# Kernel tuning notes

Measured on AMD Instinct MI355X. Metric: run time of the kernel, lower is better.

Reference implementation:

```python
import jax, jax.numpy as jnp
import numpy as np

EPS = 1e-5
NUM_GRAPHS = 64


def _linear(x, W, b):
    return x @ W + b


def setup_inputs() -> dict:
    key = jax.random.key(0)
    ks = jax.random.split(key, 32)
    N, E, IN, EF, H, ED, T, L, C = 25000, 400000, 128, 16, 32, 32, 4, 2, 1
    F = H            # F_in (divide_input=False)
    Fo = H // T      # F_out per tower

    def w(k, shape):
        return jax.random.normal(k, shape, jnp.float32) / np.sqrt(shape[-2])

    inp = {
        'x': jax.random.normal(ks[0], (N, IN), jnp.float32),
        'edge_attr': jax.random.normal(ks[1], (E, EF), jnp.float32),
        'edge_weight': jax.random.uniform(ks[2], (E,), jnp.float32),
        'edge_index': jax.random.randint(ks[3], (2, E), 0, N),
        'batch': jnp.sort(jax.random.randint(ks[4], (N,), 0, NUM_GRAPHS)),
        'node_W': w(ks[5], (IN, H)), 'node_b': jnp.zeros((H,), jnp.float32),
        'edge_W': w(ks[6], (EF, ED)), 'edge_b': jnp.zeros((ED,), jnp.float32),
        'enc_W': w(ks[7], (L, ED, F)), 'enc_b': jnp.zeros((L, F), jnp.float32),
        'pre_W': w(ks[8], (L, T, 3 * F, F)), 'pre_b': jnp.zeros((L, T, F), jnp.float32),
        'post_W': w(ks[9], (L, T, 13 * F, Fo)), 'post_b': jnp.zeros((L, T, Fo), jnp.float32),
        'lin_W': w(ks[10], (L, H, H)), 'lin_b': jnp.zeros((L, H), jnp.float32),
        'bn_g': jnp.ones((L, H), jnp.float32), 'bn_b': jnp.zeros((L, H), jnp.float32),
        'mlp_W1': w(ks[11], (H, H)), 'mlp_b1': jnp.zeros((H,), jnp.float32),
        'mlp_W2': w(ks[12], (H, H // 2)), 'mlp_b2': jnp.zeros((H // 2,), jnp.float32),
        'mlp_W3': w(ks[13], (H // 2, C)), 'mlp_b3': jnp.zeros((C,), jnp.float32),
    }
    return inp


def reference(x, edge_attr, edge_weight, node_W, node_b, edge_W, edge_b,
              enc_W, enc_b, pre_W, pre_b, post_W, post_b, lin_W, lin_b,
              bn_g, bn_b, mlp_W1, mlp_b1, mlp_W2, mlp_b2, mlp_W3, mlp_b3,
              edge_index, batch):
    N = x.shape[0]
    L, T = pre_W.shape[0], pre_W.shape[1]
    src, dst = edge_index[0], edge_index[1]

    # degree-based scalers (PNA): avg_deg_log = mean_n log(deg_n + 1)
    deg = jax.ops.segment_sum(jnp.ones((src.shape[0],), x.dtype), dst, num_segments=N)
    avg_deg_log = jnp.mean(jnp.log(deg + 1.0))
    degc = jnp.clip(deg, 1.0)[:, None, None]          # [N,1,1]
    log_deg = jnp.log(degc + 1.0)
    amp = log_deg / avg_deg_log                        # amplification scaler
    att = avg_deg_log / log_deg                        # attenuation scaler
    has_edge = (deg > 0)[:, None, None]

    h = _linear(x, node_W, node_b)                     # node_emb  [N,H]
    e = _linear(edge_attr, edge_W, edge_b)             # edge_emb  [E,ED]

    for l in range(L):
        el = _linear(e, enc_W[l], enc_b[l])            # edge_encoder [E,F]
        m_in = jnp.concatenate([h[dst], h[src], el], axis=-1)      # [E,3F]
        msg = jnp.einsum('ef,tfg->etg', m_in, pre_W[l]) + pre_b[l]  # per-tower pre_nn [E,T,F]
        msg = msg * edge_weight[:, None, None]
        s = jax.ops.segment_sum(msg, dst, num_segments=N)
        s2 = jax.ops.segment_sum(msg * msg, dst, num_segments=N)
        mean = s / degc
        std = jnp.sqrt(jax.nn.relu(s2 / degc - mean * mean) + EPS)
        mn = jnp.where(has_edge, jax.ops.segment_min(msg, dst, num_segments=N), 0.0)
        mx = jnp.where(has_edge, jax.ops.segment_max(msg, dst, num_segments=N), 0.0)
        agg = jnp.concatenate([mean, mn, mx, std], axis=-1)            # [N,T,4F]
        agg = jnp.concatenate([agg, agg * amp, agg * att], axis=-1)    # [N,T,12F]
        out = jnp.concatenate(
            [jnp.broadcast_to(h[:, None, :], (N, T, h.shape[-1])), agg], axis=-1)  # [N,T,13F]
        out = jnp.einsum('ntf,tfg->ntg', out, post_W[l]) + post_b[l]   # post_nn [N,T,Fo]
        out = out.reshape(N, -1) @ lin_W[l] + lin_b[l]                 # [N,H]
        mu = jnp.mean(out, axis=0)
        var = jnp.var(out, axis=0)
        out = (out - mu) / jnp.sqrt(var + EPS) * bn_g[l] + bn_b[l]     # BatchNorm (batch stats)
        h = jax.nn.relu(out)

    g = jax.ops.segment_sum(h, batch, num_segments=NUM_GRAPHS)        # global_add_pool
    g = jax.nn.relu(_linear(g, mlp_W1, mlp_b1))
    g = jax.nn.relu(_linear(g, mlp_W2, mlp_b2))
    return _linear(g, mlp_W3, mlp_b3)
```

## Files before the change

kernel.cpp:

```cpp
#include <hip/hip_runtime.h>

constexpr float kEps = 1e-5f;

typedef _Float16 h2 __attribute__((ext_vector_type(2)));

__device__ __forceinline__ unsigned short f2bf(float x) {
  unsigned int u = __float_as_uint(x);
  unsigned int r = (u + 0x7fffu + ((u >> 16) & 1u)) >> 16;
  return (unsigned short)r;
}
__device__ __forceinline__ float bflo(unsigned int u) { return __uint_as_float(u << 16); }
__device__ __forceinline__ float bfhi(unsigned int u) { return __uint_as_float(u & 0xffff0000u); }
__device__ __forceinline__ unsigned int packbf(float a, float b) {
  return (unsigned int)f2bf(a) | ((unsigned int)f2bf(b) << 16);
}
__device__ __forceinline__ unsigned int pkh2(float a, float b) {
  h2 v; v.x = (_Float16)a; v.y = (_Float16)b;
  return __builtin_bit_cast(unsigned int, v);
}
__device__ __forceinline__ float dot2a(h2 a, h2 b, float c) {
#if __has_builtin(__builtin_amdgcn_fdot2)
  return __builtin_amdgcn_fdot2(a, b, c, false);
#else
  return c + (float)a.x * (float)b.x + (float)a.y * (float)b.y;
#endif
}
__device__ __forceinline__ h2 ash2(unsigned int u) { return __builtin_bit_cast(h2, u); }


__global__ void zero_kernel(int* __restrict__ a, int* __restrict__ b,
                            float* __restrict__ bnb, int n) {
  int i = blockIdx.x * blockDim.x + threadIdx.x;
  if (i < n) { a[i] = 0; b[i] = 0; }
  if (i < 128) bnb[i] = 0.f;
}

__global__ void hist_kernel(const int* __restrict__ dst, int* __restrict__ deg, int E) {
  int e = blockIdx.x * blockDim.x + threadIdx.x;
  if (e < E) atomicAdd(&deg[dst[e]], 1);
}

__global__ void scan1_kernel(const int* __restrict__ deg, int* __restrict__ off,
                             int* __restrict__ part, int N) {
  __shared__ int sm[1024];
  int i = blockIdx.x * 1024 + threadIdx.x;
  int v = (i < N) ? deg[i] : 0;
  sm[threadIdx.x] = v;
  __syncthreads();
  for (int o = 1; o < 1024; o <<= 1) {
    int t = (threadIdx.x >= o) ? sm[threadIdx.x - o] : 0;
    __syncthreads();
    sm[threadIdx.x] += t;
    __syncthreads();
  }
  if (i < N) off[i] = sm[threadIdx.x] - v;
  if (threadIdx.x == 1023) part[blockIdx.x] = sm[1023];
}

__global__ void scan2_kernel(int* __restrict__ part, int* __restrict__ off, int nb, int N) {
  if (threadIdx.x == 0) {
    int run = 0;
    for (int b = 0; b < nb; b++) { int p = part[b]; part[b] = run; run += p; }
    off[N] = run;
  }
}

__global__ void scan3_kernel(int* __restrict__ off, const int* __restrict__ part, int N) {
  int i = blockIdx.x * 1024 + threadIdx.x;
  if (i < N) off[i] += part[blockIdx.x];
}

__global__ void fill_kernel(const int* __restrict__ src, const int* __restrict__ dst,
                            const float* __restrict__ ew, const float4* __restrict__ eattr4,
                            const int* __restrict__ off, int* __restrict__ cnt,
                            int* __restrict__ srcs, float* __restrict__ ews,
                            uint4* __restrict__ eg16, int E) {
  int e = blockIdx.x * blockDim.x + threadIdx.x;
  if (e < E) {
    int d = dst[e];
    int slot = off[d] + atomicAdd(&cnt[d], 1);
    srcs[slot] = src[e];
    ews[slot] = ew[e];
    float4 a = eattr4[e * 4 + 0], b = eattr4[e * 4 + 1];
    float4 c = eattr4[e * 4 + 2], q = eattr4[e * 4 + 3];
    uint4 u0, u1;
    u0.x = pkh2(a.x, a.y); u0.y = pkh2(a.z, a.w);
    u0.z = pkh2(b.x, b.y); u0.w = pkh2(b.z, b.w);
    u1.x = pkh2(c.x, c.y); u1.y = pkh2(c.z, c.w);
    u1.z = pkh2(q.x, q.y); u1.w = pkh2(q.z, q.w);
    eg16[(size_t)slot * 2 + 0] = u0;
    eg16[(size_t)slot * 2 + 1] = u1;
  }
}

__global__ void adl_kernel(const int* __restrict__ deg, float* __restrict__ adl, int N) {
  __shared__ float sm[1024];
  float s = 0.f;
  for (int n = threadIdx.x; n < N; n += 1024) s += logf((float)deg[n] + 1.f);
  sm[threadIdx.x] = s;
  __syncthreads();
  for (int o = 512; o > 0; o >>= 1) {
    if (threadIdx.x < o) sm[threadIdx.x] += sm[threadIdx.x + o];
    __syncthreads();
  }
  if (threadIdx.x == 0) adl[0] = sm[0];
}

__global__ void node_emb_kernel(const float* __restrict__ x, const float* __restrict__ W,
                                const float* __restrict__ b, float* __restrict__ h, int N) {
  int n = blockIdx.x * 8 + (threadIdx.x >> 5);
  int j = threadIdx.x & 31;
  if (n >= N) return;
  float acc = b[j];
  const float4* x4 = (const float4*)(x + (size_t)n * 128);
#pragma unroll
  for (int q = 0; q < 32; q++) {
    float4 v = x4[q];
    acc += v.x * W[(4 * q + 0) * 32 + j];
    acc += v.y * W[(4 * q + 1) * 32 + j];
    acc += v.z * W[(4 * q + 2) * 32 + j];
    acc += v.w * W[(4 * q + 3) * 32 + j];
  }
  h[n * 32 + j] = acc;
}

__global__ void fuse_kernel(const float* __restrict__ edge_W, const float* __restrict__ edge_b,
                            const float* __restrict__ enc_W, const float* __restrict__ enc_b,
                            const float* __restrict__ pre_W, const float* __restrict__ pre_b,
                            float* __restrict__ Wf, float* __restrict__ bf) {
  __shared__ float tW[2][16][32];
  __shared__ float tb[2][32];
  int tid = threadIdx.x;
  for (int i = tid; i < 1024; i += 256) {
    int l = i >> 9, r = (i >> 5) & 15, c = i & 31;
    float s = 0.f;
    for (int k = 0; k < 32; k++) s += edge_W[r * 32 + k] * enc_W[(l * 32 + k) * 32 + c];
    tW[l][r][c] = s;
  }
  for (int i = tid; i < 64; i += 256) {
    int l = i >> 5, c = i & 31;
    float s = enc_b[l * 32 + c];
    for (int k = 0; k < 32; k++) s += edge_b[k] * enc_W[(l * 32 + k) * 32 + c];
    tb[l][c] = s;
  }
  __syncthreads();
  for (int i = tid; i < 4096; i += 256) {
    int l = i >> 11, t = (i >> 9) & 3, r = (i >> 5) & 15, c = i & 31;
    float s = 0.f;
    for (int k = 0; k < 32; k++) s += tW[l][r][k] * pre_W[((l * 4 + t) * 96 + 64 + k) * 32 + c];
    Wf[i] = s;
  }
  for (int i = tid; i < 256; i += 256) {
    int l = i >> 7, t = (i >> 5) & 3, c = i & 31;
    float s = pre_b[(l * 4 + t) * 32 + c];
    for (int k = 0; k < 32; k++) s += tb[l][k] * pre_W[((l * 4 + t) * 96 + 64 + k) * 32 + c];
    bf[i] = s;
  }
}

__global__ __launch_bounds__(256) void prep_kernel(
    const float* __restrict__ h, const float* __restrict__ preW,
    const float* __restrict__ bfv, unsigned short* __restrict__ qB,
    unsigned short* __restrict__ AB, int N) {
  __shared__ float hs[16][32];
  int tid = threadIdx.x;
  int c = tid & 127, half = tid >> 7;
  int t = c >> 5, g = c & 31;
  float ws[32], wd[32];
  {
    const float* pS = preW + (t * 96 + 32) * 32 + g;
    const float* pD = preW + (t * 96) * 32 + g;
#pragma unroll
    for (int k = 0; k < 32; k++) { ws[k] = pS[k * 32]; wd[k] = pD[k * 32]; }
  }
  float bc = bfv[c];
  int base = blockIdx.x * 16;
  for (int i = tid; i < 512; i += 256) {
    int nn = i >> 5;
    hs[nn][i & 31] = (base + nn < N) ? h[(size_t)(base + nn) * 32 + (i & 31)] : 0.f;
  }
  __syncthreads();
#pragma unroll
  for (int nn = 0; nn < 8; ++nn) {
    int nl = half + 2 * nn;
    int n = base + nl;
    if (n >= N) continue;
    float qa = 0.f, Aa = bc;
#pragma unroll
    for (int k = 0; k < 32; k++) {
      float hk = hs[nl][k];
      qa = fmaf(hk, ws[k], qa);
      Aa = fmaf(hk, wd[k], Aa);
    }
    qB[(size_t)n * 128 + c] = f2bf(qa);
    AB[(size_t)n * 128 + c] = f2bf(Aa);
  }
}

__global__ __launch_bounds__(256) void bnprep_kernel(
    const float* __restrict__ pre, const float* __restrict__ bnv,
    const float* __restrict__ gamma, const float* __restrict__ beta,
    const float* __restrict__ preW, const float* __restrict__ bfv,
    float* __restrict__ h, unsigned short* __restrict__ qB,
    unsigned short* __restrict__ AB, int N) {
  __shared__ float hs[16][32];
  int tid = threadIdx.x;
  int base = blockIdx.x * 16;
  float invN = 1.f / (float)N;
  for (int idx = tid; idx < 512; idx += 256) {
    int nn = idx >> 5, j = idx & 31;
    int n = base + nn;
    float v = 0.f;
    if (n < N) {
      float mu = bnv[j] * invN;
      float var = bnv[32 + j] * invN - mu * mu;
      float is = rsqrtf(var + kEps);
      v = fmaxf((pre[(size_t)n * 32 + j] - mu) * is * gamma[j] + beta[j], 0.f);
      h[(size_t)n * 32 + j] = v;
    }
    hs[nn][j] = v;
  }
  int c = tid & 127, half = tid >> 7;
  int t = c >> 5, g = c & 31;
  float ws[32], wd[32];
  {
    const float* pS = preW + (t * 96 + 32) * 32 + g;
    const float* pD = preW + (t * 96) * 32 + g;
#pragma unroll
    for (int k = 0; k < 32; k++) { ws[k] = pS[k * 32]; wd[k] = pD[k * 32]; }
  }
  float bc = bfv[c];
  __syncthreads();
#pragma unroll
  for (int nn = 0; nn < 8; ++nn) {
    int nl = half + 2 * nn;
    int n = base + nl;
    if (n >= N) continue;
    float qa = 0.f, Aa = bc;
#pragma unroll
    for (int k = 0; k < 32; k++) {
      float hk = hs[nl][k];
      qa = fmaf(hk, ws[k], qa);
      Aa = fmaf(hk, wd[k], Aa);
    }
    qB[(size_t)n * 128 + c] = f2bf(qa);
    AB[(size_t)n * 128 + c] = f2bf(Aa);
  }
}

#define DOTE(F0, F1, UA, UB)                                         \
  F0 = dot2a(ash2(UA.x), w0[0], F0); F1 = dot2a(ash2(UA.x), w1[0], F1); \
  F0 = dot2a(ash2(UA.y), w0[1], F0); F1 = dot2a(ash2(UA.y), w1[1], F1); \
  F0 = dot2a(ash2(UA.z), w0[2], F0); F1 = dot2a(ash2(UA.z), w1[2], F1); \
  F0 = dot2a(ash2(UA.w), w0[3], F0); F1 = dot2a(ash2(UA.w), w1[3], F1); \
  F0 = dot2a(ash2(UB.x), w0[4], F0); F1 = dot2a(ash2(UB.x), w1[4], F1); \
  F0 = dot2a(ash2(UB.y), w0[5], F0); F1 = dot2a(ash2(UB.y), w1[5], F1); \
  F0 = dot2a(ash2(UB.z), w0[6], F0); F1 = dot2a(ash2(UB.z), w1[6], F1); \
  F0 = dot2a(ash2(UB.w), w0[7], F0); F1 = dot2a(ash2(UB.w), w1[7], F1);

#define STATACC(V0, V1)                                                    \
  s0a += V0; sq0 = fmaf(V0, V0, sq0); mn0 = fminf(mn0, V0); mx0 = fmaxf(mx0, V0); \
  s1a += V1; sq1 = fmaf(V1, V1, sq1); mn1 = fminf(mn1, V1); mx1 = fmaxf(mx1, V1);

__global__ __launch_bounds__(256, 4) void agg8_kernel(
    const unsigned int* __restrict__ qB, const unsigned int* __restrict__ AB,
    const int* __restrict__ coff, const int* __restrict__ srcs,
    const float* __restrict__ ews, const uint4* __restrict__ eg16,
    const float* __restrict__ Wf, unsigned int* __restrict__ stats, int N) {
  int lane = threadIdx.x & 63;
  int n = (blockIdx.x * blockDim.x + threadIdx.x) >> 6;
  if (n >= N) return;
  int t = lane >> 4, g0 = (2 * lane) & 31;
  h2 w0[8], w1[8];
  {
    const float* p = Wf + t * 512 + g0;
#pragma unroll
    for (int k = 0; k < 8; k++) {
      w0[k].x = (_Float16)p[(2 * k) * 32];     w0[k].y = (_Float16)p[(2 * k + 1) * 32];
      w1[k].x = (_Float16)p[(2 * k) * 32 + 1]; w1[k].y = (_Float16)p[(2 * k + 1) * 32 + 1];
    }
  }
  unsigned int au = AB[(size_t)n * 64 + lane];
  float a0 = bflo(au), a1 = bfhi(au);
  int beg = coff[n], end = coff[n + 1];
  int dg = end - beg;
  float s0a = 0.f, s1a = 0.f, sq0 = 0.f, sq1 = 0.f;
  float mn0 = 1e30f, mn1 = 1e30f, mx0 = -1e30f, mx1 = -1e30f;

  int i = beg;
  int sc0 = 0, sc1 = 0, sc2 = 0, sc3 = 0;
  if (i + 4 <= end) { sc0 = srcs[i]; sc1 = srcs[i + 1]; sc2 = srcs[i + 2]; sc3 = srcs[i + 3]; }
  for (; i + 4 <= end; i += 4) {
    unsigned int q0 = qB[(size_t)sc0 * 64 + lane];
    unsigned int q1 = qB[(size_t)sc1 * 64 + lane];
    unsigned int q2 = qB[(size_t)sc2 * 64 + lane];
    unsigned int q3 = qB[(size_t)sc3 * 64 + lane];
    float w0s = ews[i], w1s = ews[i + 1], w2s = ews[i + 2], w3s = ews[i + 3];
    const uint4* ep = eg16 + (size_t)i * 2;
    uint4 eA0 = ep[0], eA1 = ep[1], eB0 = ep[2], eB1 = ep[3];
    uint4 eC0 = ep[4], eC1 = ep[5], eD0 = ep[6], eD1 = ep[7];
    if (i + 8 <= end) { sc0 = srcs[i + 4]; sc1 = srcs[i + 5]; sc2 = srcs[i + 6]; sc3 = srcs[i + 7]; }
    float f00 = 0.f, f10 = 0.f, f01 = 0.f, f11 = 0.f;
    float f02 = 0.f, f12 = 0.f, f03 = 0.f, f13 = 0.f;
    DOTE(f00, f10, eA0, eA1)
    DOTE(f01, f11, eB0, eB1)
    DOTE(f02, f12, eC0, eC1)
    DOTE(f03, f13, eD0, eD1)
    float v0, v1;
    v0 = (a0 + bflo(q0) + f00) * w0s; v1 = (a1 + bfhi(q0) + f10) * w0s; STATACC(v0, v1)
    v0 = (a0 + bflo(q1) + f01) * w1s; v1 = (a1 + bfhi(q1) + f11) * w1s; STATACC(v0, v1)
    v0 = (a0 + bflo(q2) + f02) * w2s; v1 = (a1 + bfhi(q2) + f12) * w2s; STATACC(v0, v1)
    v0 = (a0 + bflo(q3) + f03) * w3s; v1 = (a1 + bfhi(q3) + f13) * w3s; STATACC(v0, v1)
  }
  for (; i < end; ++i) {
    int s = srcs[i];
    unsigned int q = qB[(size_t)s * 64 + lane];
    float w = ews[i];
    const uint4* ep = eg16 + (size_t)i * 2;
    uint4 ea = ep[0], eb = ep[1];
    float f0 = 0.f, f1 = 0.f;
    DOTE(f0, f1, ea, eb)
    float v0 = (a0 + bflo(q) + f0) * w;
    float v1 = (a1 + bfhi(q) + f1) * w;
    STATACC(v0, v1)
  }
  if (dg == 0) { mn0 = 0.f; mx0 = 0.f; mn1 = 0.f; mx1 = 0.f; }
  float inv = 1.f / (float)(dg > 0 ? dg : 1);
  float mean0 = s0a * inv, mean1 = s1a * inv;
  float sd0 = sqrtf(fmaxf(sq0 * inv - mean0 * mean0, 0.f) + kEps);
  float sd1 = sqrtf(fmaxf(sq1 * inv - mean1 * mean1, 0.f) + kEps);
  unsigned int* sp = stats + (size_t)n * 256;
  sp[0 * 64 + lane] = packbf(mean0, mean1);
  sp[1 * 64 + lane] = packbf(mn0, mn1);
  sp[2 * 64 + lane] = packbf(mx0, mx1);
  sp[3 * 64 + lane] = packbf(sd0, sd1);
}

__global__ __launch_bounds__(256) void post_kernel(
    const float* __restrict__ h, const unsigned int* __restrict__ stats,
    const int* __restrict__ coff, const float* __restrict__ adl,
    const float* __restrict__ postW, const float* __restrict__ postB,
    const float* __restrict__ linW, const float* __restrict__ linB,
    float* __restrict__ pre, float* __restrict__ bn, int N) {
  __shared__ unsigned int pwp[208 * 32];
  __shared__ unsigned int stu[4][256];
  __shared__ float red[8][32];
  int tid = threadIdx.x;
  for (int i = tid; i < 6656; i += 256) {
    int r = i >> 5, cc = i & 31, tP = cc >> 3, gq = cc & 7;
    float lo = postW[tP * 3328 + (2 * r) * 8 + gq];
    float hi = postW[tP * 3328 + (2 * r + 1) * 8 + gq];
    pwp[i] = packbf(lo, hi);
  }
  __syncthreads();

  int wave = tid >> 6, lane = tid & 63;
  int c = lane & 31, hh = lane >> 5;
  int tP = c >> 3;
  float adN = adl[0];
  float bs = 0.f, bq = 0.f;

  for (int n = blockIdx.x * 4 + wave; n < N; n += gridDim.x * 4) {
    {
      uint4 su = ((const uint4*)stats)[(size_t)n * 64 + lane];
      ((uint4*)stu[wave])[lane] = su;
    }
    int dg = coff[n + 1] - coff[n];
    float degc = (float)(dg > 0 ? dg : 1);
    float ad = adN / (float)N;
    float ld = logf(degc + 1.f);
    float amp = ld / ad, att = ad / ld;

    float acc = (hh == 0) ? postB[tP * 8 + (c & 7)] : 0.f;
    const float4* h4 = (const float4*)(h + (size_t)n * 32);
#pragma unroll
    for (int q4 = 0; q4 < 4; q4++) {
      float4 hv = h4[hh * 4 + q4];
      int r0 = hh * 8 + q4 * 2;
      unsigned int u0 = pwp[r0 * 32 + c], u1 = pwp[(r0 + 1) * 32 + c];
      acc = fmaf(hv.x, bflo(u0), acc);
      acc = fmaf(hv.y, bfhi(u0), acc);
      acc = fmaf(hv.z, bflo(u1), acc);
      acc = fmaf(hv.w, bfhi(u1), acc);
    }
#pragma unroll 8
    for (int jj = 0; jj < 32; jj++) {
      int sIdx = hh * 2 + (jj >> 4);
      unsigned int sv = stu[wave][sIdx * 64 + tP * 16 + (jj & 15)];
      float v0 = bflo(sv), v1 = bfhi(sv);
      int rm = 16 + hh * 32 + jj, ra = 80 + hh * 32 + jj, rt = 144 + hh * 32 + jj;
      unsigned int um = pwp[rm * 32 + c];
      unsigned int ua = pwp[ra * 32 + c];
      unsigned int ut = pwp[rt * 32 + c];
      float w0 = bflo(um); w0 = fmaf(amp, bflo(ua), w0); w0 = fmaf(att, bflo(ut), w0);
      float w1 = bfhi(um); w1 = fmaf(amp, bfhi(ua), w1); w1 = fmaf(att, bfhi(ut), w1);
      acc = fmaf(v0, w0, acc);
      acc = fmaf(v1, w1, acc);
    }
    acc += __shfl_xor(acc, 32);
    float o = linB[c];
#pragma unroll
    for (int k = 0; k < 32; k++) {
      float a = __shfl(acc, k);
      o = fmaf(a, linW[k * 32 + c], o);
    }
    if (lane < 32) {
      pre[(size_t)n * 32 + c] = o;
      bs += o;
      bq = fmaf(o, o, bq);
    }
  }

  __syncthreads();
  if (lane < 32) {
    red[wave * 2 + 0][c] = bs;
    red[wave * 2 + 1][c] = bq;
  }
  __syncthreads();
  if (tid < 64) {
    int which = tid >> 5, cc = tid & 31;
    float s = red[0 * 2 + which][cc] + red[1 * 2 + which][cc] +
              red[2 * 2 + which][cc] + red[3 * 2 + which][cc];
    atomicAdd(&bn[which * 32 + cc], s);
  }
}


__device__ __forceinline__ int lower_bound_dev(const int* a, int n, int key) {
  int lo = 0, hi = n;
  while (lo < hi) {
    int m = (lo + hi) >> 1;
    if (a[m] < key) lo = m + 1; else hi = m;
  }
  return lo;
}

__global__ void pool2_kernel(const float* __restrict__ pre, const float* __restrict__ bnv,
                             const float* __restrict__ gamma, const float* __restrict__ beta,
                             const int* __restrict__ batch, float* __restrict__ gp, int N) {
  int gi = blockIdx.x;
  int lo = lower_bound_dev(batch, N, gi);
  int hi = lower_bound_dev(batch, N, gi + 1);
  __shared__ float part[8][32];
  int j = threadIdx.x & 31, ch = threadIdx.x >> 5;
  float invN = 1.f / (float)N;
  float mu = bnv[j] * invN;
  float var = bnv[32 + j] * invN - mu * mu;
  float is = rsqrtf(var + kEps);
  float gm = gamma[j], bt = beta[j];
  float s = 0.f;
  for (int n = lo + ch; n < hi; n += 8)
    s += fmaxf((pre[(size_t)n * 32 + j] - mu) * is * gm + bt, 0.f);
  part[ch][j] = s;
  __syncthreads();
  if (threadIdx.x < 32) {
    float t = 0.f;
    for (int c2 = 0; c2 < 8; c2++) t += part[c2][j];
    gp[gi * 32 + j] = t;
  }
}

__global__ void mlp_kernel(const float* __restrict__ gp,
                           const float* __restrict__ W1, const float* __restrict__ b1,
                           const float* __restrict__ W2, const float* __restrict__ b2,
                           const float* __restrict__ W3, const float* __restrict__ b3,
                           float* __restrict__ out) {
  __shared__ float g1[64 * 32];
  __shared__ float g2[64 * 16];
  int tid = threadIdx.x;
  for (int i = tid; i < 2048; i += 256) {
    int r = i >> 5, c = i & 31;
    float s = b1[c];
    for (int k = 0; k < 32; k++) s += gp[r * 32 + k] * W1[k * 32 + c];
    g1[i] = fmaxf(s, 0.f);
  }
  __syncthreads();
  for (int i = tid; i < 1024; i += 256) {
    int r = i >> 4, c = i & 15;
    float s = b2[c];
    for (int k = 0; k < 32; k++) s += g1[r * 32 + k] * W2[k * 16 + c];
    g2[i] = fmaxf(s, 0.f);
  }
  __syncthreads();
  if (tid < 64) {
    float s = b3[0];
    for (int k = 0; k < 16; k++) s += g2[tid * 16 + k] * W3[k];
    out[tid] = s;
  }
}


extern "C" void kernel_launch(void* const* d_in, const int* in_sizes, int n_in,
                              void* d_out, int out_size, void* d_ws, size_t ws_size,
                              hipStream_t stream) {
  (void)n_in; (void)out_size; (void)ws_size;
  const float* x     = (const float*)d_in[0];
  const float* eattr = (const float*)d_in[1];
  const float* ew    = (const float*)d_in[2];
  const int*   eidx  = (const int*)d_in[3];
  const int*   batch = (const int*)d_in[4];
  const float* nodeW = (const float*)d_in[5];
  const float* nodeB = (const float*)d_in[6];
  const float* edgeW = (const float*)d_in[7];
  const float* edgeB = (const float*)d_in[8];
  const float* encW  = (const float*)d_in[9];
  const float* encB  = (const float*)d_in[10];
  const float* preW  = (const float*)d_in[11];
  const float* preB  = (const float*)d_in[12];
  const float* postW = (const float*)d_in[13];
  const float* postB = (const float*)d_in[14];
  const float* linW  = (const float*)d_in[15];
  const float* linB  = (const float*)d_in[16];
  const float* bnG   = (const float*)d_in[17];
  const float* bnB   = (const float*)d_in[18];
  const float* W1    = (const float*)d_in[19];
  const float* b1    = (const float*)d_in[20];
  const float* W2    = (const float*)d_in[21];
  const float* b2    = (const float*)d_in[22];
  const float* W3    = (const float*)d_in[23];
  const float* b3    = (const float*)d_in[24];
  float* out = (float*)d_out;

  int N = in_sizes[0] / 128;
  int E = in_sizes[2];
  const int* srcp = eidx;
  const int* dstp = eidx + E;

  char* wsb = (char*)d_ws;
  size_t woff = 0;
  auto alloc = [&](size_t bytes) -> void* {
    void* p = (void*)(wsb + woff);
    woff += (bytes + 255) & ~(size_t)255;
    return p;
  };
  int* deg   = (int*)alloc((size_t)N * 4);
  int* cnt   = (int*)alloc((size_t)N * 4);
  int* coff  = (int*)alloc((size_t)(N + 1) * 4);
  int* part  = (int*)alloc(64 * 4);
  int* srcs  = (int*)alloc((size_t)E * 4);
  float* ews = (float*)alloc((size_t)E * 4);
  unsigned int* eg16 = (unsigned int*)alloc((size_t)E * 32);
  float* h    = (float*)alloc((size_t)N * 32 * 4);
  float* pre  = (float*)alloc((size_t)N * 32 * 4);
  float* adl  = (float*)alloc(256);
  float* bnbuf = (float*)alloc(2 * 64 * 4);
  float* gp   = (float*)alloc(64 * 32 * 4);
  float* WfB  = (float*)alloc(2 * 4 * 16 * 32 * 4);
  float* bfB  = (float*)alloc(2 * 4 * 32 * 4);
  unsigned short* qB  = (unsigned short*)alloc((size_t)N * 128 * 2);
  unsigned short* AB  = (unsigned short*)alloc((size_t)N * 128 * 2);
  unsigned int* stats = (unsigned int*)alloc((size_t)N * 256 * 4);

  int nb = (N + 1023) / 1024;
  zero_kernel<<<(N + 255) / 256, 256, 0, stream>>>(deg, cnt, bnbuf, N);
  hist_kernel<<<(E + 255) / 256, 256, 0, stream>>>(dstp, deg, E);
  scan1_kernel<<<nb, 1024, 0, stream>>>(deg, coff, part, N);
  scan2_kernel<<<1, 64, 0, stream>>>(part, coff, nb, N);
  scan3_kernel<<<nb, 1024, 0, stream>>>(coff, part, N);
  fill_kernel<<<(E + 255) / 256, 256, 0, stream>>>(srcp, dstp, ew, (const float4*)eattr,
                                                   coff, cnt, srcs, ews, (uint4*)eg16, E);
  adl_kernel<<<1, 1024, 0, stream>>>(deg, adl, N);
  node_emb_kernel<<<(N + 7) / 8, 256, 0, stream>>>(x, nodeW, nodeB, h, N);
  fuse_kernel<<<1, 256, 0, stream>>>(edgeW, edgeB, encW, encB, preW, preB, WfB, bfB);

  prep_kernel<<<(N + 15) / 16, 256, 0, stream>>>(h, preW, bfB, qB, AB, N);
  agg8_kernel<<<(N + 3) / 4, 256, 0, stream>>>(
      (const unsigned int*)qB, (const unsigned int*)AB, coff, srcs, ews,
      (const uint4*)eg16, WfB, stats, N);
  post_kernel<<<1280, 256, 0, stream>>>(
      h, stats, coff, adl, postW, postB, linW, linB, pre, bnbuf, N);
  bnprep_kernel<<<(N + 15) / 16, 256, 0, stream>>>(
      pre, bnbuf, bnG, bnB, preW + 12288, bfB + 128, h, qB, AB, N);
  agg8_kernel<<<(N + 3) / 4, 256, 0, stream>>>(
      (const unsigned int*)qB, (const unsigned int*)AB, coff, srcs, ews,
      (const uint4*)eg16, WfB + 2048, stats, N);
  post_kernel<<<1280, 256, 0, stream>>>(
      h, stats, coff, adl, postW + 13312, postB + 32, linW + 1024, linB + 32,
      pre, bnbuf + 64, N);
  pool2_kernel<<<64, 256, 0, stream>>>(pre, bnbuf + 64, bnG + 32, bnB + 32, batch, gp, N);
  mlp_kernel<<<1, 256, 0, stream>>>(gp, W1, b1, W2, b2, W3, b3, out);
}
```

Measured before the change: 388.6 us.

## Prefetch neighbor rows one iteration ahead and pack post-kernel scaler FMAs

The aggregation kernel now issues the gathers of source-node rows for the next group of four edges before computing the current group, and fetches source indices two groups ahead. The aim is to hide gather latency behind the edge dot-product math. The post kernel keeps three packed two-wide accumulators (mean, amplified, attenuated) and applies the amp and att scalers once at the end instead of per term, which cuts per-iteration FMAs. Its grid is also halved. The prefetch raises register pressure and the reordered sums can change rounding slightly.

```diff
diff --git a/kernel.cpp b/kernel.cpp
--- a/kernel.cpp
+++ b/kernel.cpp
@@ -3,6 +3,7 @@
 constexpr float kEps = 1e-5f;
 
 typedef _Float16 h2 __attribute__((ext_vector_type(2)));
+typedef float f2v __attribute__((ext_vector_type(2)));
 
 __device__ __forceinline__ unsigned short f2bf(float x) {
   unsigned int u = __float_as_uint(x);
@@ -26,6 +27,8 @@
 #endif
 }
 __device__ __forceinline__ h2 ash2(unsigned int u) { return __builtin_bit_cast(h2, u); }
+__device__ __forceinline__ f2v fma2(f2v a, f2v b, f2v c) { return __builtin_elementwise_fma(a, b, c); }
+__device__ __forceinline__ f2v unbf2(unsigned int u) { f2v r; r.x = bflo(u); r.y = bfhi(u); return r; }
 
 
 __global__ void zero_kernel(int* __restrict__ a, int* __restrict__ b,
@@ -262,7 +265,7 @@
   s0a += V0; sq0 = fmaf(V0, V0, sq0); mn0 = fminf(mn0, V0); mx0 = fmaxf(mx0, V0); \
   s1a += V1; sq1 = fmaf(V1, V1, sq1); mn1 = fminf(mn1, V1); mx1 = fmaxf(mx1, V1);
 
-__global__ __launch_bounds__(256, 4) void agg8_kernel(
+__global__ __launch_bounds__(256, 4) void agg9_kernel(
     const unsigned int* __restrict__ qB, const unsigned int* __restrict__ AB,
     const int* __restrict__ coff, const int* __restrict__ srcs,
     const float* __restrict__ ews, const uint4* __restrict__ eg16,
@@ -288,18 +291,29 @@
   float mn0 = 1e30f, mn1 = 1e30f, mx0 = -1e30f, mx1 = -1e30f;
 
   int i = beg;
+  unsigned int q0 = 0, q1 = 0, q2 = 0, q3 = 0;
   int sc0 = 0, sc1 = 0, sc2 = 0, sc3 = 0;
-  if (i + 4 <= end) { sc0 = srcs[i]; sc1 = srcs[i + 1]; sc2 = srcs[i + 2]; sc3 = srcs[i + 3]; }
+  if (i + 4 <= end) {
+    int t0 = srcs[i], t1 = srcs[i + 1], t2 = srcs[i + 2], t3 = srcs[i + 3];
+    q0 = qB[(size_t)t0 * 64 + lane];
+    q1 = qB[(size_t)t1 * 64 + lane];
+    q2 = qB[(size_t)t2 * 64 + lane];
+    q3 = qB[(size_t)t3 * 64 + lane];
+  }
+  if (i + 8 <= end) { sc0 = srcs[i + 4]; sc1 = srcs[i + 5]; sc2 = srcs[i + 6]; sc3 = srcs[i + 7]; }
   for (; i + 4 <= end; i += 4) {
-    unsigned int q0 = qB[(size_t)sc0 * 64 + lane];
-    unsigned int q1 = qB[(size_t)sc1 * 64 + lane];
-    unsigned int q2 = qB[(size_t)sc2 * 64 + lane];
-    unsigned int q3 = qB[(size_t)sc3 * 64 + lane];
+    unsigned int nq0 = 0, nq1 = 0, nq2 = 0, nq3 = 0;
+    if (i + 8 <= end) {
+      nq0 = qB[(size_t)sc0 * 64 + lane];
+      nq1 = qB[(size_t)sc1 * 64 + lane];
+      nq2 = qB[(size_t)sc2 * 64 + lane];
+      nq3 = qB[(size_t)sc3 * 64 + lane];
+    }
     float w0s = ews[i], w1s = ews[i + 1], w2s = ews[i + 2], w3s = ews[i + 3];
     const uint4* ep = eg16 + (size_t)i * 2;
     uint4 eA0 = ep[0], eA1 = ep[1], eB0 = ep[2], eB1 = ep[3];
     uint4 eC0 = ep[4], eC1 = ep[5], eD0 = ep[6], eD1 = ep[7];
-    if (i + 8 <= end) { sc0 = srcs[i + 4]; sc1 = srcs[i + 5]; sc2 = srcs[i + 6]; sc3 = srcs[i + 7]; }
+    if (i + 12 <= end) { sc0 = srcs[i + 8]; sc1 = srcs[i + 9]; sc2 = srcs[i + 10]; sc3 = srcs[i + 11]; }
     float f00 = 0.f, f10 = 0.f, f01 = 0.f, f11 = 0.f;
     float f02 = 0.f, f12 = 0.f, f03 = 0.f, f13 = 0.f;
     DOTE(f00, f10, eA0, eA1)
@@ -311,6 +325,7 @@
     v0 = (a0 + bflo(q1) + f01) * w1s; v1 = (a1 + bfhi(q1) + f11) * w1s; STATACC(v0, v1)
     v0 = (a0 + bflo(q2) + f02) * w2s; v1 = (a1 + bfhi(q2) + f12) * w2s; STATACC(v0, v1)
     v0 = (a0 + bflo(q3) + f03) * w3s; v1 = (a1 + bfhi(q3) + f13) * w3s; STATACC(v0, v1)
+    q0 = nq0; q1 = nq1; q2 = nq2; q3 = nq3;
   }
   for (; i < end; ++i) {
     int s = srcs[i];
@@ -383,20 +398,24 @@
       acc = fmaf(hv.z, bflo(u1), acc);
       acc = fmaf(hv.w, bfhi(u1), acc);
     }
+    f2v ym, ya, yt;
+    ym.x = 0.f; ym.y = 0.f; ya = ym; yt = ym;
 #pragma unroll 8
     for (int jj = 0; jj < 32; jj++) {
       int sIdx = hh * 2 + (jj >> 4);
       unsigned int sv = stu[wave][sIdx * 64 + tP * 16 + (jj & 15)];
-      float v0 = bflo(sv), v1 = bfhi(sv);
-      int rm = 16 + hh * 32 + jj, ra = 80 + hh * 32 + jj, rt = 144 + hh * 32 + jj;
-      unsigned int um = pwp[rm * 32 + c];
-      unsigned int ua = pwp[ra * 32 + c];
-      unsigned int ut = pwp[rt * 32 + c];
-      float w0 = bflo(um); w0 = fmaf(amp, bflo(ua), w0); w0 = fmaf(att, bflo(ut), w0);
-      float w1 = bfhi(um); w1 = fmaf(amp, bfhi(ua), w1); w1 = fmaf(att, bfhi(ut), w1);
-      acc = fmaf(v0, w0, acc);
-      acc = fmaf(v1, w1, acc);
-    }
+      f2v v2 = unbf2(sv);
+      int rm = 16 + hh * 32 + jj;
+      f2v um = unbf2(pwp[rm * 32 + c]);
+      f2v ua = unbf2(pwp[(rm + 64) * 32 + c]);
+      f2v ut = unbf2(pwp[(rm + 128) * 32 + c]);
+      ym = fma2(v2, um, ym);
+      ya = fma2(v2, ua, ya);
+      yt = fma2(v2, ut, yt);
+    }
+    acc += ym.x + ym.y;
+    acc = fmaf(amp, ya.x + ya.y, acc);
+    acc = fmaf(att, yt.x + yt.y, acc);
     acc += __shfl_xor(acc, 32);
     float o = linB[c];
 #pragma unroll
@@ -564,17 +583,17 @@
   fuse_kernel<<<1, 256, 0, stream>>>(edgeW, edgeB, encW, encB, preW, preB, WfB, bfB);
 
   prep_kernel<<<(N + 15) / 16, 256, 0, stream>>>(h, preW, bfB, qB, AB, N);
-  agg8_kernel<<<(N + 3) / 4, 256, 0, stream>>>(
+  agg9_kernel<<<(N + 3) / 4, 256, 0, stream>>>(
       (const unsigned int*)qB, (const unsigned int*)AB, coff, srcs, ews,
       (const uint4*)eg16, WfB, stats, N);
-  post_kernel<<<1280, 256, 0, stream>>>(
+  post_kernel<<<640, 256, 0, stream>>>(
       h, stats, coff, adl, postW, postB, linW, linB, pre, bnbuf, N);
   bnprep_kernel<<<(N + 15) / 16, 256, 0, stream>>>(
       pre, bnbuf, bnG, bnB, preW + 12288, bfB + 128, h, qB, AB, N);
-  agg8_kernel<<<(N + 3) / 4, 256, 0, stream>>>(
+  agg9_kernel<<<(N + 3) / 4, 256, 0, stream>>>(
       (const unsigned int*)qB, (const unsigned int*)AB, coff, srcs, ews,
       (const uint4*)eg16, WfB + 2048, stats, N);
-  post_kernel<<<1280, 256, 0, stream>>>(
+  post_kernel<<<640, 256, 0, stream>>>(
       h, stats, coff, adl, postW + 13312, postB + 32, linW + 1024, linB + 32,
       pre, bnbuf + 64, N);
   pool2_kernel<<<64, 256, 0, stream>>>(pre, bnbuf + 64, bnG + 32, bnB + 32, batch, gp, N);
```

Result: faster. 377.6 us (-2.8%).
